# Optimization experiments

Hardware: AMD Instinct MI355X
Metric: run time of the kernel (lower is better)

The kernel has to match this reference:

```python
import jax, jax.numpy as jnp
import numpy as np

DECAY = 0.99
EPS = 1e-5  # Laplace smoothing eps in cluster-size balancing


def _quantize(z_flat, embedding, cluster_size, emb_avg, n_codes):
    # z_flat: [N, D]; embedding: [K, D]
    d = (jnp.sum(z_flat * z_flat, axis=1, keepdims=True)
         + jnp.sum(embedding * embedding, axis=1)
         - 2.0 * (z_flat @ embedding.T))                      # [N, K]
    idx = jnp.argmin(d, axis=1)                               # [N]
    # EMA update (training path). segment_sum == one-hot matmul scatter-add.
    counts = jax.ops.segment_sum(jnp.ones(z_flat.shape[0], z_flat.dtype), idx,
                                 num_segments=n_codes)        # [K]
    new_cs = cluster_size * DECAY + (1.0 - DECAY) * counts
    dw = jax.ops.segment_sum(z_flat, idx, num_segments=n_codes)  # [K, D]
    new_avg = emb_avg * DECAY + (1.0 - DECAY) * dw
    n = new_cs.sum()
    bal = (new_cs + EPS) / (n + n_codes * EPS) * n
    # torch assigns via .data (no autograd) -> stop_gradient for faithfulness
    new_emb = jax.lax.stop_gradient(new_avg / bal[:, None])
    z_q = jnp.take(new_emb, idx, axis=0)  # == one_hot(idx) @ new_emb
    return idx, z_q


def _l2norm(x):
    # F.normalize(x, dim=-1) with eps=1e-12
    return x / jnp.maximum(jnp.linalg.norm(x, axis=-1, keepdims=True), 1e-12)


def reference(z, structure_embedding, style_embedding,
              structure_cluster_size, style_cluster_size,
              structure_embedding_avg, style_embedding_avg):
    b, c, h, w, d = z.shape
    zp = jnp.transpose(z, (0, 2, 3, 4, 1))      # b h w d c
    z_flat = zp.reshape(-1, c)                  # [N, D]
    s_idx, s_q = _quantize(z_flat, structure_embedding, structure_cluster_size,
                           structure_embedding_avg, structure_embedding.shape[0])
    y_idx, y_q = _quantize(z_flat, style_embedding, style_cluster_size,
                           style_embedding_avg, style_embedding.shape[0])

    def back(q):  # [N, C] -> b c h w d
        return jnp.transpose(q.reshape(b, h, w, d, c), (0, 4, 1, 2, 3))

    s_enc = back(s_q)
    y_enc = back(y_q)
    # NOTE: faithful to source — normalize over LAST axis of (b,c,h,w,d),
    # i.e. the spatial depth axis, exactly as F.normalize(dim=-1) does there.
    dis = jnp.mean(jnp.sum(_l2norm(s_enc) * _l2norm(y_enc), axis=-1) ** 2)
    z_q = (s_enc + y_enc) * 0.5
    return z_q, dis, s_idx, y_idx


def setup_inputs() -> dict:
    key = jax.random.key(0)
    k1, k2, k3 = jax.random.split(key, 3)
    B, C, H, W, D = 16, 256, 16, 16, 16
    Ks, Ky = 1024, 512
    return {
        "z": jax.random.normal(k1, (B, C, H, W, D), dtype=jnp.float32),
        "structure_embedding": jax.random.normal(k2, (Ks, C), dtype=jnp.float32),
        "style_embedding": jax.random.normal(k3, (Ky, C), dtype=jnp.float32),
        "structure_cluster_size": jnp.zeros((Ks,), jnp.float32),
        "style_cluster_size": jnp.zeros((Ky,), jnp.float32),
        "structure_embedding_avg": jnp.zeros((Ks, C), jnp.float32),
        "style_embedding_avg": jnp.zeros((Ky, C), jnp.float32),
    }
```

## Files before the change

### kernel.cpp

```cpp
#include <hip/hip_runtime.h>
#include <float.h>

#define NROWS 65536
#define CDIM  256
#define KS    1024
#define KY    512
#define KTOT  1536
#define SPB   4096

#define WB_CNT_S       0
#define WB_CNT_Y       4096
#define WB_RESCUE_CNT  6144
#define WB_DISACC      6152
#define WB_DW_S        6400
#define WB_DW_Y        1054976
#define WB_ZERO_BYTES  1579264
#define WB_EIMG        1579264
#define WB_EN2         2365696
#define WB_IDXS_I      2371840
#define WB_IDXY_I      2633984
#define WB_RLIST_S     2896128
#define WB_RLIST_Y     3158272
#define WB_BASE_S      3420416
#define WB_BASE_Y      3424512
#define WB_CUR_S       3426560
#define WB_CUR_Y       3430656
#define WB_SCALE_S     3432704
#define WB_SCALE_Y     3436800
#define WB_PERM_S      3438848
#define WB_PERM_Y      3700992
#define WB_KSORT_S     3963136
#define WB_KSORT_Y     4225280
#define WB_EMB_S       4487424
#define WB_EMB_Y       5536000

#define OFF_OUT_ZQ   0
#define OFF_OUT_DIS  16777216
#define OFF_OUT_SIDX 16777217
#define OFF_OUT_YIDX 16842753

typedef __attribute__((ext_vector_type(8)))  _Float16 f16x8;
typedef __attribute__((ext_vector_type(4)))  float    f32x4;

__device__ __forceinline__ unsigned int umn(unsigned int a, unsigned int b) { return a < b ? a : b; }
__device__ __forceinline__ unsigned int umx(unsigned int a, unsigned int b) { return a > b ? a : b; }

__global__ void prep_e(const float* __restrict__ Es, const float* __restrict__ Ey,
                       unsigned short* __restrict__ eimg, float* __restrict__ en2) {
    int k = blockIdx.x;
    int lane = threadIdx.x;
    const float* E = (k < KS) ? (Es + (size_t)k * CDIM) : (Ey + (size_t)(k - KS) * CDIM);
    float4 v = *(const float4*)(E + lane * 4);
    float nrm = v.x * v.x + v.y * v.y + v.z * v.z + v.w * v.w;
#pragma unroll
    for (int off = 32; off > 0; off >>= 1) nrm += __shfl_down(nrm, off);
    if (lane == 0) en2[k] = nrm;

    unsigned short q0 = __builtin_bit_cast(unsigned short, (_Float16)v.x);
    unsigned short q1 = __builtin_bit_cast(unsigned short, (_Float16)v.y);
    unsigned short q2 = __builtin_bit_cast(unsigned short, (_Float16)v.z);
    unsigned short q3 = __builtin_bit_cast(unsigned short, (_Float16)v.w);
    uint2 hp = make_uint2((unsigned)q0 | ((unsigned)q1 << 16),
                          (unsigned)q2 | ((unsigned)q3 << 16));

    int c0 = lane * 4;
    int kc = c0 >> 5, g = (c0 >> 3) & 3, j0 = c0 & 7;
    size_t byteoff = (size_t)(k >> 4) * 8192 + (size_t)kc * 1024
                   + (size_t)(g * 16 + (k & 15)) * 16 + (size_t)j0 * 2;
    *(uint2*)((char*)eimg + byteoff) = hp;
}

__global__ void prep_z(const float* __restrict__ z, float* __restrict__ zf) {
    __shared__ float Zs[32][257];
    int blk = blockIdx.x;
    int n0 = blk * 32, b = n0 >> 12, s0 = n0 & 4095;
    int t = threadIdx.x;
    const float* zb = z + (size_t)b * CDIM * SPB + s0;
#pragma unroll
    for (int i = 0; i < 32; ++i) {
        int l = i * 256 + t;
        int c = l >> 5, s = l & 31;
        Zs[s][c] = zb[(size_t)c * SPB + s];
    }
    __syncthreads();
#pragma unroll
    for (int j = 0; j < 8; ++j) {
        int gid = j * 256 + t;
        int nl = gid >> 6, fg = gid & 63;
        float4 v = *(const float4*)(&Zs[nl][fg * 4]);
        *(float4*)(&zf[(size_t)(n0 + nl) * 256 + fg * 4]) = v;
    }
}

__device__ __forceinline__ void stage4(const unsigned short* __restrict__ eimg,
                                       int chunk, char* lsbase, int wrow, int lane) {
    const char* gs = (const char*)eimg + (size_t)chunk * 8192 + wrow * 4096 + lane * 16;
    char* ls = lsbase + wrow * 4096;
#pragma unroll
    for (int i = 0; i < 4; ++i)
        __builtin_amdgcn_global_load_lds(
            (const __attribute__((address_space(1))) void*)(gs + i * 1024),
            (__attribute__((address_space(3))) void*)(ls + i * 1024), 16, 0, 0);
}

__launch_bounds__(256, 3)
__global__ void assign_kernel(const float* __restrict__ zf, const unsigned short* __restrict__ eimg,
                              const float* __restrict__ en2,
                              float* __restrict__ sidx_f, float* __restrict__ yidx_f,
                              int* __restrict__ sidx_i, int* __restrict__ yidx_i,
                              int* __restrict__ cnt_s, int* __restrict__ cnt_y,
                              int* __restrict__ rescue_cnt,
                              int* __restrict__ rlist_s, int* __restrict__ rlist_y) {
    __shared__ char shraw[32768];
    __shared__ unsigned int mv1[64], mv2[64];
    const int tid = threadIdx.x, wave = tid >> 6, lane = tid & 63;
    const int pair = wave >> 1, wrow = wave & 1;
    const int n0 = blockIdx.x * 64;
    char* shp = shraw + pair * 16384;

    stage4(eimg, pair * 48, shp, wrow, lane);

    f16x8 A[2][8];
#pragma unroll
    for (int rg = 0; rg < 2; ++rg) {
        const float* zr = zf + (size_t)(n0 + wrow * 32 + rg * 16 + (lane & 15)) * 256
                        + (lane >> 4) * 8;
#pragma unroll
        for (int kc = 0; kc < 8; ++kc) {
            float4 f0 = *(const float4*)(zr + kc * 32);
            float4 f1 = *(const float4*)(zr + kc * 32 + 4);
            f16x8 a;
            a[0] = (_Float16)f0.x; a[1] = (_Float16)f0.y;
            a[2] = (_Float16)f0.z; a[3] = (_Float16)f0.w;
            a[4] = (_Float16)f1.x; a[5] = (_Float16)f1.y;
            a[6] = (_Float16)f1.z; a[7] = (_Float16)f1.w;
            A[rg][kc] = a;
        }
    }

    unsigned int m1a[2][4], m2a[2][4];
#pragma unroll
    for (int rg = 0; rg < 2; ++rg)
#pragma unroll
        for (int q = 0; q < 4; ++q) { m1a[rg][q] = 0xFFFFFFFFu; m2a[rg][q] = 0xFFFFFFFFu; }

    for (int i = 0; i < 48; ++i) {
        const int chunk = pair * 48 + i;
        if (i + 1 < 48) {
            stage4(eimg, chunk + 1, shp + ((i + 1) & 1) * 8192, wrow, lane);
            asm volatile("s_waitcnt vmcnt(4)" ::: "memory");
        } else {
            asm volatile("s_waitcnt vmcnt(0)" ::: "memory");
        }
        __builtin_amdgcn_s_barrier();
        asm volatile("" ::: "memory");

        const char* bb = shp + (i & 1) * 8192 + lane * 16;
        f32x4 acc0 = {}, acc1 = {};
#pragma unroll
        for (int kc = 0; kc < 8; ++kc) {
            f16x8 B = *(const f16x8*)(bb + kc * 1024);
            acc0 = __builtin_amdgcn_mfma_f32_16x16x32_f16(A[0][kc], B, acc0, 0, 0, 0);
            acc1 = __builtin_amdgcn_mfma_f32_16x16x32_f16(A[1][kc], B, acc1, 0, 0, 0);
        }
        const int kcode = chunk * 16 + (lane & 15);
        const float en0 = en2[kcode] + 512.0f;
        const unsigned int tag = (unsigned int)kcode;
#pragma unroll
        for (int q = 0; q < 4; ++q) {
            float d0 = fmaf(-2.f, acc0[q], en0);
            unsigned int du0 = (__float_as_uint(d0) & 0xFFFFF800u) | tag;
            m2a[0][q] = umn(m2a[0][q], umx(m1a[0][q], du0));
            m1a[0][q] = umn(m1a[0][q], du0);
            float d1 = fmaf(-2.f, acc1[q], en0);
            unsigned int du1 = (__float_as_uint(d1) & 0xFFFFF800u) | tag;
            m2a[1][q] = umn(m2a[1][q], umx(m1a[1][q], du1));
            m1a[1][q] = umn(m1a[1][q], du1);
        }
        asm volatile("s_waitcnt lgkmcnt(0)" ::: "memory");
        __builtin_amdgcn_s_barrier();
        asm volatile("" ::: "memory");

        if (pair == 1 && i == 15) {
#pragma unroll
            for (int rg = 0; rg < 2; ++rg)
#pragma unroll
                for (int q = 0; q < 4; ++q) {
                    unsigned int v1 = m1a[rg][q], v2 = m2a[rg][q];
#pragma unroll
                    for (int m = 8; m >= 1; m >>= 1) {
                        unsigned int o1 = (unsigned int)__shfl_xor((int)v1, m);
                        unsigned int o2 = (unsigned int)__shfl_xor((int)v2, m);
                        v2 = umn(umn(v2, o2), umx(v1, o1));
                        v1 = umn(v1, o1);
                    }
                    if ((lane & 15) == 0) {
                        int r64 = wrow * 32 + rg * 16 + (lane >> 4) * 4 + q;
                        mv1[r64] = v1; mv2[r64] = v2;
                    }
                    m1a[rg][q] = 0xFFFFFFFFu; m2a[rg][q] = 0xFFFFFFFFu;
                }
        }
    }

    if (pair == 0) {
#pragma unroll
        for (int rg = 0; rg < 2; ++rg)
#pragma unroll
            for (int q = 0; q < 4; ++q) {
                unsigned int v1 = m1a[rg][q], v2 = m2a[rg][q];
#pragma unroll
                for (int m = 8; m >= 1; m >>= 1) {
                    unsigned int o1 = (unsigned int)__shfl_xor((int)v1, m);
                    unsigned int o2 = (unsigned int)__shfl_xor((int)v2, m);
                    v2 = umn(umn(v2, o2), umx(v1, o1));
                    v1 = umn(v1, o1);
                }
                if ((lane & 15) == 0) {
                    int r64 = wrow * 32 + rg * 16 + (lane >> 4) * 4 + q;
                    unsigned int p1 = mv1[r64], p2 = mv2[r64];
                    unsigned int nv2 = umn(umn(v2, p2), umx(v1, p1));
                    unsigned int nv1 = umn(v1, p1);
                    int kw = (int)(nv1 & 0x7FFu);
                    int n = n0 + r64;
                    sidx_f[n] = (float)kw;
                    sidx_i[n] = kw;
                    atomicAdd(&cnt_s[kw], 1);
                    if ((nv1 >> 11) + 4 > (nv2 >> 11)) {
                        int k2w = (int)(nv2 & 0x7FFu);
                        int p = atomicAdd(&rescue_cnt[0], 1);
                        if (p < 65536) rlist_s[p] = n | (k2w << 16);
                    }
                }
            }
    } else {
#pragma unroll
        for (int rg = 0; rg < 2; ++rg)
#pragma unroll
            for (int q = 0; q < 4; ++q) {
                unsigned int v1 = m1a[rg][q], v2 = m2a[rg][q];
#pragma unroll
                for (int m = 8; m >= 1; m >>= 1) {
                    unsigned int o1 = (unsigned int)__shfl_xor((int)v1, m);
                    unsigned int o2 = (unsigned int)__shfl_xor((int)v2, m);
                    v2 = umn(umn(v2, o2), umx(v1, o1));
                    v1 = umn(v1, o1);
                }
                if ((lane & 15) == 0) {
                    int r64 = wrow * 32 + rg * 16 + (lane >> 4) * 4 + q;
                    int kw = (int)(v1 & 0x7FFu) - KS;
                    int n = n0 + r64;
                    yidx_f[n] = (float)kw;
                    yidx_i[n] = kw;
                    atomicAdd(&cnt_y[kw], 1);
                    if ((v1 >> 11) + 4 > (v2 >> 11)) {
                        int k2w = (int)(v2 & 0x7FFu) - KS;
                        int p = atomicAdd(&rescue_cnt[1], 1);
                        if (p < 65536) rlist_y[p] = n | (k2w << 16);
                    }
                }
            }
    }
}

__global__ void rescue2_kernel(const float* __restrict__ zf,
                               const float* __restrict__ Es, const float* __restrict__ Ey,
                               const float* __restrict__ en2, const int* __restrict__ rcnt,
                               const int* __restrict__ rlist_s, const int* __restrict__ rlist_y,
                               float* __restrict__ sidx_f, float* __restrict__ yidx_f,
                               int* __restrict__ sidx_i, int* __restrict__ yidx_i,
                               int* __restrict__ cnt_s, int* __restrict__ cnt_y) {
    int cs = rcnt[0]; if (cs > 65536) cs = 65536;
    int cy = rcnt[1]; if (cy > 65536) cy = 65536;
    int total = cs + cy;
    const int lane = threadIdx.x & 63;
    const int nw = (gridDim.x * blockDim.x) >> 6;
    for (int e = (int)((blockIdx.x * blockDim.x + threadIdx.x) >> 6); e < total; e += nw) {
        int book = (e >= cs);
        unsigned int ent = (unsigned int)(book ? rlist_y[e - cs] : rlist_s[e]);
        int n  = (int)(ent & 0xFFFFu);
        int k2 = (int)(ent >> 16);
        int* idx_i = book ? yidx_i : sidx_i;
        float* idx_f = book ? yidx_f : sidx_f;
        int* cnt = book ? cnt_y : cnt_s;
        const float* E = book ? Ey : Es;
        const float* en2k = book ? (en2 + KS) : en2;
        int k1 = idx_i[n];
        float4 zv = *(const float4*)(zf + (size_t)n * 256 + lane * 4);
        float4 a  = *(const float4*)(E + (size_t)k1 * 256 + lane * 4);
        float4 c  = *(const float4*)(E + (size_t)k2 * 256 + lane * 4);
        float d1 = zv.x * a.x + zv.y * a.y + zv.z * a.z + zv.w * a.w;
        float d2 = zv.x * c.x + zv.y * c.y + zv.z * c.z + zv.w * c.w;
#pragma unroll
        for (int off = 32; off > 0; off >>= 1) {
            d1 += __shfl_down(d1, off);
            d2 += __shfl_down(d2, off);
        }
        if (lane == 0) {
            float dist1 = en2k[k1] - 2.f * d1;
            float dist2 = en2k[k2] - 2.f * d2;
            int nk = (dist2 < dist1 || (dist2 == dist1 && k2 < k1)) ? k2 : k1;
            if (nk != k1) {
                atomicSub(&cnt[k1], 1);
                atomicAdd(&cnt[nk], 1);
                idx_i[n] = nk;
                idx_f[n] = (float)nk;
            }
        }
    }
}

__global__ void scanbal_kernel(const float* __restrict__ cs_in, const float* __restrict__ cy_in,
                               const int* __restrict__ cnt_s, const int* __restrict__ cnt_y,
                               int* __restrict__ base_s, int* __restrict__ base_y,
                               int* __restrict__ cur_s, int* __restrict__ cur_y,
                               float* __restrict__ scale_s, float* __restrict__ scale_y) {
    __shared__ int   sc[1024];
    __shared__ float sf[1024];
    int K = blockIdx.x ? KY : KS;
    const float* csi = blockIdx.x ? cy_in : cs_in;
    const int*   cnt = blockIdx.x ? cnt_y : cnt_s;
    int* base = blockIdx.x ? base_y : base_s;
    int* cur  = blockIdx.x ? cur_y  : cur_s;
    float* scale = blockIdx.x ? scale_y : scale_s;
    int t = threadIdx.x;
    int c = (t < K) ? cnt[t] : 0;
    float ncs = (t < K) ? (csi[t] * 0.99f + 0.01f * (float)c) : 0.f;
    sc[t] = c;
    __syncthreads();
    for (int off = 1; off < 1024; off <<= 1) {
        int v = sc[t] + ((t >= off) ? sc[t - off] : 0);
        __syncthreads();
        sc[t] = v;
        __syncthreads();
    }
    int incl = sc[t];
    sf[t] = ncs;
    __syncthreads();
    for (int s2 = 512; s2 > 0; s2 >>= 1) {
        if (t < s2) sf[t] += sf[t + s2];
        __syncthreads();
    }
    float nsum = sf[0];
    if (t < K) {
        base[t] = incl - c;
        cur[t]  = incl - c;
        float bal = (ncs + 1e-5f) / (nsum + (float)K * 1e-5f) * nsum;
        scale[t] = 1.0f / bal;
    }
}

__global__ void scatter_kernel(const int* __restrict__ si, const int* __restrict__ yi,
                               int* __restrict__ cur_s, int* __restrict__ cur_y,
                               int* __restrict__ perm_s, int* __restrict__ perm_y,
                               int* __restrict__ ksort_s, int* __restrict__ ksort_y) {
    int i = blockIdx.x * 256 + threadIdx.x;
    if (i < NROWS) {
        int k = si[i]; int p = atomicAdd(&cur_s[k], 1);
        perm_s[p] = i; ksort_s[p] = k;
    } else {
        int n = i - NROWS; int k = yi[n]; int p = atomicAdd(&cur_y[k], 1);
        perm_y[p] = n; ksort_y[p] = k;
    }
}

__global__ void dw_kernel(const float* __restrict__ zf,
                          const int* __restrict__ perm_s, const int* __restrict__ ksort_s,
                          const int* __restrict__ perm_y, const int* __restrict__ ksort_y,
                          float* __restrict__ dw_s, float* __restrict__ dw_y) {
    __shared__ int keys[33];
    __shared__ int rows[32];
    const int t = threadIdx.x;
    int blk = blockIdx.x;
    const int* perm; const int* ks; float* dw; int p0;
    if (blk < NROWS / 32) { perm = perm_s; ks = ksort_s; dw = dw_s; p0 = blk * 32; }
    else                  { perm = perm_y; ks = ksort_y; dw = dw_y; p0 = (blk - NROWS / 32) * 32; }
    if (t < 32) { keys[t] = ks[p0 + t]; rows[t] = perm[p0 + t]; }
    if (t == 32) keys[32] = -1;
    __syncthreads();
    float acc = 0.f;
#pragma unroll 8
    for (int j = 0; j < 32; ++j) {
        acc += zf[(size_t)rows[j] * 256 + t];
        if (keys[j + 1] != keys[j]) {
            atomicAdd(&dw[(size_t)keys[j] * 256 + t], acc);
            acc = 0.f;
        }
    }
}

__global__ void embnew_kernel(const float* __restrict__ avg_s, const float* __restrict__ avg_y,
                              const float* __restrict__ dw_s, const float* __restrict__ dw_y,
                              const float* __restrict__ scale_s, const float* __restrict__ scale_y,
                              float* __restrict__ emb_s, float* __restrict__ emb_y) {
    int id = blockIdx.x, t = threadIdx.x;
    if (id < KS) { int i = id * 256 + t; emb_s[i] = (avg_s[i] * 0.99f + 0.01f * dw_s[i]) * scale_s[id]; }
    else { int kk = id - KS; int i = kk * 256 + t; emb_y[i] = (avg_y[i] * 0.99f + 0.01f * dw_y[i]) * scale_y[kk]; }
}

__global__ void gather_kernel(const float* __restrict__ Se, const float* __restrict__ Ye,
                              const int* __restrict__ sidx, const int* __restrict__ yidx,
                              float* __restrict__ zq, float* __restrict__ disacc) {
    __shared__ float qb[256 * 17];
    __shared__ int   si[16], yi[16];
    __shared__ float red[256];
    const int g  = blockIdx.x;
    const int b  = g >> 8;
    const int hw = g & 255;
    const int t  = threadIdx.x;
    if (t < 16) {
        int n = b * SPB + hw * 16 + t;
        si[t] = sidx[n];
        yi[t] = yidx[n];
    }
    __syncthreads();
    float ns = 0.f, ny = 0.f, dot = 0.f;
#pragma unroll
    for (int d = 0; d < 16; ++d) {
        float s = Se[(size_t)si[d] * CDIM + t];
        float y = Ye[(size_t)yi[d] * CDIM + t];
        ns  = fmaf(s, s, ns);
        ny  = fmaf(y, y, ny);
        dot = fmaf(s, y, dot);
        qb[t * 17 + d] = 0.5f * (s + y);
    }
    float den = fmaxf(sqrtf(ns), 1e-12f) * fmaxf(sqrtf(ny), 1e-12f);
    float val = dot / den;
    red[t] = val * val;
    __syncthreads();
    for (int s = 128; s > 0; s >>= 1) {
        if (t < s) red[t] += red[t + s];
        __syncthreads();
    }
    if (t == 0) atomicAdd(disacc, red[0]);
    float* zg = zq + (size_t)b * CDIM * SPB + hw * 16;
#pragma unroll
    for (int j = 0; j < 16; ++j) {
        int e = j * 256 + t;
        int c = e >> 4, d = e & 15;
        zg[(size_t)c * SPB + d] = qb[c * 17 + d];
    }
}

__global__ void fin_kernel(const float* __restrict__ disacc, float* __restrict__ out_dis) {
    *out_dis = *disacc * (1.0f / 1048576.0f);
}

extern "C" void kernel_launch(void* const* d_in, const int* in_sizes, int n_in,
                              void* d_out, int out_size, void* d_ws, size_t ws_size,
                              hipStream_t stream) {
    const float* z     = (const float*)d_in[0];
    const float* Es    = (const float*)d_in[1];
    const float* Ey    = (const float*)d_in[2];
    const float* s_cs  = (const float*)d_in[3];
    const float* y_cs  = (const float*)d_in[4];
    const float* s_avg = (const float*)d_in[5];
    const float* y_avg = (const float*)d_in[6];
    float* out = (float*)d_out;
    char*  w   = (char*)d_ws;

    unsigned short* eimg = (unsigned short*)(w + WB_EIMG);
    float* en2    = (float*)(w + WB_EN2);
    int* idxs_i   = (int*)(w + WB_IDXS_I);
    int* idxy_i   = (int*)(w + WB_IDXY_I);
    int* cnt_s    = (int*)(w + WB_CNT_S);
    int* cnt_y    = (int*)(w + WB_CNT_Y);
    int* r_cnt    = (int*)(w + WB_RESCUE_CNT);
    int* rlist_s  = (int*)(w + WB_RLIST_S);
    int* rlist_y  = (int*)(w + WB_RLIST_Y);
    int* base_s   = (int*)(w + WB_BASE_S);
    int* base_y   = (int*)(w + WB_BASE_Y);
    int* cur_s    = (int*)(w + WB_CUR_S);
    int* cur_y    = (int*)(w + WB_CUR_Y);
    float* scale_s = (float*)(w + WB_SCALE_S);
    float* scale_y = (float*)(w + WB_SCALE_Y);
    int* perm_s   = (int*)(w + WB_PERM_S);
    int* perm_y   = (int*)(w + WB_PERM_Y);
    int* ksort_s  = (int*)(w + WB_KSORT_S);
    int* ksort_y  = (int*)(w + WB_KSORT_Y);
    float* dw_s   = (float*)(w + WB_DW_S);
    float* dw_y   = (float*)(w + WB_DW_Y);
    float* emb_s  = (float*)(w + WB_EMB_S);
    float* emb_y  = (float*)(w + WB_EMB_Y);

    float* zf     = out + OFF_OUT_ZQ;
    float* sidx_f = out + OFF_OUT_SIDX;
    float* yidx_f = out + OFF_OUT_YIDX;

    hipMemsetAsync(w, 0, WB_ZERO_BYTES, stream);

    prep_e<<<KTOT, 64, 0, stream>>>(Es, Ey, eimg, en2);
    prep_z<<<NROWS / 32, 256, 0, stream>>>(z, zf);

    assign_kernel<<<NROWS / 64, 256, 0, stream>>>(zf, eimg, en2, sidx_f, yidx_f,
                                                  idxs_i, idxy_i, cnt_s, cnt_y,
                                                  r_cnt, rlist_s, rlist_y);

    rescue2_kernel<<<512, 256, 0, stream>>>(zf, Es, Ey, en2, r_cnt, rlist_s, rlist_y,
                                            sidx_f, yidx_f, idxs_i, idxy_i, cnt_s, cnt_y);

    scanbal_kernel<<<2, 1024, 0, stream>>>(s_cs, y_cs, cnt_s, cnt_y, base_s, base_y,
                                           cur_s, cur_y, scale_s, scale_y);
    scatter_kernel<<<2 * NROWS / 256, 256, 0, stream>>>(idxs_i, idxy_i, cur_s, cur_y,
                                                        perm_s, perm_y, ksort_s, ksort_y);
    dw_kernel<<<2 * NROWS / 32, 256, 0, stream>>>(zf, perm_s, ksort_s, perm_y, ksort_y, dw_s, dw_y);
    embnew_kernel<<<KTOT, 256, 0, stream>>>(s_avg, y_avg, dw_s, dw_y, scale_s, scale_y, emb_s, emb_y);
    gather_kernel<<<4096, 256, 0, stream>>>(emb_s, emb_y, idxs_i, idxy_i,
                                            out + OFF_OUT_ZQ, (float*)(w + WB_DISACC));
    fin_kernel<<<1, 1, 0, stream>>>((float*)(w + WB_DISACC), out + OFF_OUT_DIS);
}
```

Measured before the change: 322.2 us.

## Restructure assign kernel into 8-wave blocks sharing a 4-deep LDS codebook pipeline

The assign kernel changes from 256-thread blocks of 64 rows, where two wave pairs each scanned half the codebook, to 512-thread blocks of 256 rows. In the new layout every wave owns 32 rows and scans all 1536 codes. Codebook tiles of 32 codes are staged cooperatively by all 8 waves into a 4-slot LDS ring with a prefetch distance of two. Each staged tile now serves 256 rows instead of 32, which cuts global and L2 traffic for the codebook. The cross-pair merge through shared memory goes away, at the cost of more registers per wave, lower occupancy bounds, only 256 blocks, and a single barrier per phase that relies on a 4-deep ring to avoid overwrite hazards.

```diff
diff --git a/kernel.cpp b/kernel.cpp
--- a/kernel.cpp
+++ b/kernel.cpp
@@ -92,18 +92,18 @@
     }
 }
 
-__device__ __forceinline__ void stage4(const unsigned short* __restrict__ eimg,
-                                       int chunk, char* lsbase, int wrow, int lane) {
-    const char* gs = (const char*)eimg + (size_t)chunk * 8192 + wrow * 4096 + lane * 16;
-    char* ls = lsbase + wrow * 4096;
-#pragma unroll
-    for (int i = 0; i < 4; ++i)
+__device__ __forceinline__ void stage_phase(const unsigned short* __restrict__ eimg,
+                                            int phase, char* lsbase, int wave, int lane) {
+    const char* gs = (const char*)eimg + (size_t)phase * 16384 + (size_t)(wave * 2) * 1024 + lane * 16;
+    char* ls = lsbase + wave * 2 * 1024;
+#pragma unroll
+    for (int i = 0; i < 2; ++i)
         __builtin_amdgcn_global_load_lds(
             (const __attribute__((address_space(1))) void*)(gs + i * 1024),
             (__attribute__((address_space(3))) void*)(ls + i * 1024), 16, 0, 0);
 }
 
-__launch_bounds__(256, 3)
+__launch_bounds__(512, 2)
 __global__ void assign_kernel(const float* __restrict__ zf, const unsigned short* __restrict__ eimg,
                               const float* __restrict__ en2,
                               float* __restrict__ sidx_f, float* __restrict__ yidx_f,
@@ -111,19 +111,14 @@
                               int* __restrict__ cnt_s, int* __restrict__ cnt_y,
                               int* __restrict__ rescue_cnt,
                               int* __restrict__ rlist_s, int* __restrict__ rlist_y) {
-    __shared__ char shraw[32768];
-    __shared__ unsigned int mv1[64], mv2[64];
+    __shared__ char sh[4][16384];
     const int tid = threadIdx.x, wave = tid >> 6, lane = tid & 63;
-    const int pair = wave >> 1, wrow = wave & 1;
-    const int n0 = blockIdx.x * 64;
-    char* shp = shraw + pair * 16384;
-
-    stage4(eimg, pair * 48, shp, wrow, lane);
+    const int n0 = blockIdx.x * 256;
 
     f16x8 A[2][8];
 #pragma unroll
     for (int rg = 0; rg < 2; ++rg) {
-        const float* zr = zf + (size_t)(n0 + wrow * 32 + rg * 16 + (lane & 15)) * 256
+        const float* zr = zf + (size_t)(n0 + wave * 32 + rg * 16 + (lane & 15)) * 256
                         + (lane >> 4) * 8;
 #pragma unroll
         for (int kc = 0; kc < 8; ++kc) {
@@ -138,50 +133,50 @@
         }
     }
 
+    stage_phase(eimg, 0, &sh[0][0], wave, lane);
+    stage_phase(eimg, 1, &sh[1][0], wave, lane);
+
     unsigned int m1a[2][4], m2a[2][4];
 #pragma unroll
     for (int rg = 0; rg < 2; ++rg)
 #pragma unroll
         for (int q = 0; q < 4; ++q) { m1a[rg][q] = 0xFFFFFFFFu; m2a[rg][q] = 0xFFFFFFFFu; }
 
-    for (int i = 0; i < 48; ++i) {
-        const int chunk = pair * 48 + i;
-        if (i + 1 < 48) {
-            stage4(eimg, chunk + 1, shp + ((i + 1) & 1) * 8192, wrow, lane);
-            asm volatile("s_waitcnt vmcnt(4)" ::: "memory");
-        } else {
-            asm volatile("s_waitcnt vmcnt(0)" ::: "memory");
-        }
+    for (int p = 0; p < 48; ++p) {
+        if (p + 2 < 48) stage_phase(eimg, p + 2, &sh[(p + 2) & 3][0], wave, lane);
+        if (p < 46)       asm volatile("s_waitcnt vmcnt(4)" ::: "memory");
+        else if (p == 46) asm volatile("s_waitcnt vmcnt(2)" ::: "memory");
+        else              asm volatile("s_waitcnt vmcnt(0)" ::: "memory");
         __builtin_amdgcn_s_barrier();
         asm volatile("" ::: "memory");
 
-        const char* bb = shp + (i & 1) * 8192 + lane * 16;
-        f32x4 acc0 = {}, acc1 = {};
-#pragma unroll
-        for (int kc = 0; kc < 8; ++kc) {
-            f16x8 B = *(const f16x8*)(bb + kc * 1024);
-            acc0 = __builtin_amdgcn_mfma_f32_16x16x32_f16(A[0][kc], B, acc0, 0, 0, 0);
-            acc1 = __builtin_amdgcn_mfma_f32_16x16x32_f16(A[1][kc], B, acc1, 0, 0, 0);
-        }
-        const int kcode = chunk * 16 + (lane & 15);
-        const float en0 = en2[kcode] + 512.0f;
-        const unsigned int tag = (unsigned int)kcode;
-#pragma unroll
-        for (int q = 0; q < 4; ++q) {
-            float d0 = fmaf(-2.f, acc0[q], en0);
-            unsigned int du0 = (__float_as_uint(d0) & 0xFFFFF800u) | tag;
-            m2a[0][q] = umn(m2a[0][q], umx(m1a[0][q], du0));
-            m1a[0][q] = umn(m1a[0][q], du0);
-            float d1 = fmaf(-2.f, acc1[q], en0);
-            unsigned int du1 = (__float_as_uint(d1) & 0xFFFFF800u) | tag;
-            m2a[1][q] = umn(m2a[1][q], umx(m1a[1][q], du1));
-            m1a[1][q] = umn(m1a[1][q], du1);
-        }
-        asm volatile("s_waitcnt lgkmcnt(0)" ::: "memory");
-        __builtin_amdgcn_s_barrier();
-        asm volatile("" ::: "memory");
-
-        if (pair == 1 && i == 15) {
+#pragma unroll
+        for (int c = 0; c < 2; ++c) {
+            const char* cb = &sh[p & 3][c * 8192] + lane * 16;
+            f32x4 acc0 = {}, acc1 = {};
+#pragma unroll
+            for (int kc = 0; kc < 8; ++kc) {
+                f16x8 B = *(const f16x8*)(cb + kc * 1024);
+                acc0 = __builtin_amdgcn_mfma_f32_16x16x32_f16(A[0][kc], B, acc0, 0, 0, 0);
+                acc1 = __builtin_amdgcn_mfma_f32_16x16x32_f16(A[1][kc], B, acc1, 0, 0, 0);
+            }
+            const int kcode = p * 32 + c * 16 + (lane & 15);
+            const float en0 = en2[kcode] + 512.0f;
+            const unsigned int tag = (unsigned int)kcode;
+#pragma unroll
+            for (int q = 0; q < 4; ++q) {
+                float d0 = fmaf(-2.f, acc0[q], en0);
+                unsigned int du0 = (__float_as_uint(d0) & 0xFFFFF800u) | tag;
+                m2a[0][q] = umn(m2a[0][q], umx(m1a[0][q], du0));
+                m1a[0][q] = umn(m1a[0][q], du0);
+                float d1 = fmaf(-2.f, acc1[q], en0);
+                unsigned int du1 = (__float_as_uint(d1) & 0xFFFFF800u) | tag;
+                m2a[1][q] = umn(m2a[1][q], umx(m1a[1][q], du1));
+                m1a[1][q] = umn(m1a[1][q], du1);
+            }
+        }
+
+        if (p == 31) {
 #pragma unroll
             for (int rg = 0; rg < 2; ++rg)
 #pragma unroll
@@ -195,72 +190,47 @@
                         v1 = umn(v1, o1);
                     }
                     if ((lane & 15) == 0) {
-                        int r64 = wrow * 32 + rg * 16 + (lane >> 4) * 4 + q;
-                        mv1[r64] = v1; mv2[r64] = v2;
+                        int kw = (int)(v1 & 0x7FFu);
+                        int n = n0 + wave * 32 + rg * 16 + (lane >> 4) * 4 + q;
+                        sidx_f[n] = (float)kw;
+                        sidx_i[n] = kw;
+                        atomicAdd(&cnt_s[kw], 1);
+                        if ((v1 >> 11) + 4 > (v2 >> 11)) {
+                            int k2w = (int)(v2 & 0x7FFu);
+                            int pp = atomicAdd(&rescue_cnt[0], 1);
+                            if (pp < 65536) rlist_s[pp] = n | (k2w << 16);
+                        }
                     }
                     m1a[rg][q] = 0xFFFFFFFFu; m2a[rg][q] = 0xFFFFFFFFu;
                 }
         }
     }
 
-    if (pair == 0) {
-#pragma unroll
-        for (int rg = 0; rg < 2; ++rg)
-#pragma unroll
-            for (int q = 0; q < 4; ++q) {
-                unsigned int v1 = m1a[rg][q], v2 = m2a[rg][q];
-#pragma unroll
-                for (int m = 8; m >= 1; m >>= 1) {
-                    unsigned int o1 = (unsigned int)__shfl_xor((int)v1, m);
-                    unsigned int o2 = (unsigned int)__shfl_xor((int)v2, m);
-                    v2 = umn(umn(v2, o2), umx(v1, o1));
-                    v1 = umn(v1, o1);
-                }
-                if ((lane & 15) == 0) {
-                    int r64 = wrow * 32 + rg * 16 + (lane >> 4) * 4 + q;
-                    unsigned int p1 = mv1[r64], p2 = mv2[r64];
-                    unsigned int nv2 = umn(umn(v2, p2), umx(v1, p1));
-                    unsigned int nv1 = umn(v1, p1);
-                    int kw = (int)(nv1 & 0x7FFu);
-                    int n = n0 + r64;
-                    sidx_f[n] = (float)kw;
-                    sidx_i[n] = kw;
-                    atomicAdd(&cnt_s[kw], 1);
-                    if ((nv1 >> 11) + 4 > (nv2 >> 11)) {
-                        int k2w = (int)(nv2 & 0x7FFu);
-                        int p = atomicAdd(&rescue_cnt[0], 1);
-                        if (p < 65536) rlist_s[p] = n | (k2w << 16);
-                    }
+#pragma unroll
+    for (int rg = 0; rg < 2; ++rg)
+#pragma unroll
+        for (int q = 0; q < 4; ++q) {
+            unsigned int v1 = m1a[rg][q], v2 = m2a[rg][q];
+#pragma unroll
+            for (int m = 8; m >= 1; m >>= 1) {
+                unsigned int o1 = (unsigned int)__shfl_xor((int)v1, m);
+                unsigned int o2 = (unsigned int)__shfl_xor((int)v2, m);
+                v2 = umn(umn(v2, o2), umx(v1, o1));
+                v1 = umn(v1, o1);
+            }
+            if ((lane & 15) == 0) {
+                int kw = (int)(v1 & 0x7FFu) - KS;
+                int n = n0 + wave * 32 + rg * 16 + (lane >> 4) * 4 + q;
+                yidx_f[n] = (float)kw;
+                yidx_i[n] = kw;
+                atomicAdd(&cnt_y[kw], 1);
+                if ((v1 >> 11) + 4 > (v2 >> 11)) {
+                    int k2w = (int)(v2 & 0x7FFu) - KS;
+                    int pp = atomicAdd(&rescue_cnt[1], 1);
+                    if (pp < 65536) rlist_y[pp] = n | (k2w << 16);
                 }
             }
-    } else {
-#pragma unroll
-        for (int rg = 0; rg < 2; ++rg)
-#pragma unroll
-            for (int q = 0; q < 4; ++q) {
-                unsigned int v1 = m1a[rg][q], v2 = m2a[rg][q];
-#pragma unroll
-                for (int m = 8; m >= 1; m >>= 1) {
-                    unsigned int o1 = (unsigned int)__shfl_xor((int)v1, m);
-                    unsigned int o2 = (unsigned int)__shfl_xor((int)v2, m);
-                    v2 = umn(umn(v2, o2), umx(v1, o1));
-                    v1 = umn(v1, o1);
-                }
-                if ((lane & 15) == 0) {
-                    int r64 = wrow * 32 + rg * 16 + (lane >> 4) * 4 + q;
-                    int kw = (int)(v1 & 0x7FFu) - KS;
-                    int n = n0 + r64;
-                    yidx_f[n] = (float)kw;
-                    yidx_i[n] = kw;
-                    atomicAdd(&cnt_y[kw], 1);
-                    if ((v1 >> 11) + 4 > (v2 >> 11)) {
-                        int k2w = (int)(v2 & 0x7FFu) - KS;
-                        int p = atomicAdd(&rescue_cnt[1], 1);
-                        if (p < 65536) rlist_y[p] = n | (k2w << 16);
-                    }
-                }
-            }
-    }
+        }
 }
 
 __global__ void rescue2_kernel(const float* __restrict__ zf,
@@ -492,9 +462,9 @@
     prep_e<<<KTOT, 64, 0, stream>>>(Es, Ey, eimg, en2);
     prep_z<<<NROWS / 32, 256, 0, stream>>>(z, zf);
 
-    assign_kernel<<<NROWS / 64, 256, 0, stream>>>(zf, eimg, en2, sidx_f, yidx_f,
-                                                  idxs_i, idxy_i, cnt_s, cnt_y,
-                                                  r_cnt, rlist_s, rlist_y);
+    assign_kernel<<<NROWS / 256, 512, 0, stream>>>(zf, eimg, en2, sidx_f, yidx_f,
+                                                   idxs_i, idxy_i, cnt_s, cnt_y,
+                                                   r_cnt, rlist_s, rlist_y);
 
     rescue2_kernel<<<512, 256, 0, stream>>>(zf, Es, Ey, en2, r_cnt, rlist_s, rlist_y,
                                             sidx_f, yidx_f, idxs_i, idxy_i, cnt_s, cnt_y);
```

Result: no change. 327.7 us (+1.7%).
